# Kernel optimization log

Measured on AMD Instinct MI355X. Metric: run time of the kernel, lower is better.

Reference implementation:

```python
import jax, jax.numpy as jnp
import numpy as np


def _fwht(x):
    """Fast Walsh-Hadamard transform along the last axis (length must be 2^k)."""
    orig_shape = x.shape
    n = orig_shape[-1]
    x = x.reshape(-1, n)
    h = 1
    while h < n:
        # split last dim into (n // (2h), 2, h) blocks and do the butterfly
        x = x.reshape(-1, n // (2 * h), 2, h)
        a = x[:, :, 0, :]
        b = x[:, :, 1, :]
        x = jnp.stack([a + b, a - b], axis=2).reshape(-1, n)
        h *= 2
    return x.reshape(orig_shape)


def setup_inputs() -> dict:
    key = jax.random.key(0)
    x = jax.random.normal(key, (16384, 4096), dtype=jnp.float32)
    scale = jnp.ones((), dtype=jnp.float32)
    return {"x": x, "scale": scale}


def reference(x, scale):
    # Faithful to fwht(input, scale): Hadamard butterfly then scalar scale.
    return _fwht(x) * scale
```

## Files before the change

kernel.cpp:

```cpp
#include <hip/hip_runtime.h>


#define SJ 68
#define SC 1096
#define LDS_WORDS (3 * SC + 15 * SJ + 64)

__global__ __launch_bounds__(64) void fwht_kernel(
    const float* __restrict__ x, const float* __restrict__ scale,
    float* __restrict__ out) {
  __shared__ float lds[LDS_WORDS];
  const int t = threadIdx.x;
  const int row = blockIdx.x;
  const float* xr = x + (size_t)row * 4096;
  float* outr = out + (size_t)row * 4096;

  float v[16][4];
#pragma unroll
  for (int j = 0; j < 16; ++j) {
    const float4 f = *reinterpret_cast<const float4*>(xr + j * 256 + 4 * t);
    v[j][0] = f.x; v[j][1] = f.y; v[j][2] = f.z; v[j][3] = f.w;
  }

#pragma unroll
  for (int j = 0; j < 16; ++j) {
    {
      float a = v[j][0], b = v[j][1];
      v[j][0] = a + b; v[j][1] = a - b;
      float a2 = v[j][2], b2 = v[j][3];
      v[j][2] = a2 + b2; v[j][3] = a2 - b2;
    }
    {
      float a = v[j][0], b = v[j][2];
      v[j][0] = a + b; v[j][2] = a - b;
      float a2 = v[j][1], b2 = v[j][3];
      v[j][1] = a2 + b2; v[j][3] = a2 - b2;
    }
  }

#pragma unroll
  for (int bit = 0; bit < 4; ++bit) {
    const int mask = 1 << bit;
#pragma unroll
    for (int j = 0; j < 16; ++j) {
      if (!(j & mask)) {
        const int k = j | mask;
#pragma unroll
        for (int c = 0; c < 4; ++c) {
          float a = v[j][c], b = v[k][c];
          v[j][c] = a + b; v[k][c] = a - b;
        }
      }
    }
  }

#pragma unroll
  for (int j = 0; j < 16; ++j) {
#pragma unroll
    for (int c = 0; c < 4; ++c) {
      lds[t + j * SJ + c * SC] = v[j][c];
    }
  }

  __syncthreads();

  const int jp = t >> 2, cp = t & 3;
  const int rbase = jp * SJ + cp * SC;
  float w[64];
#pragma unroll
  for (int k = 0; k < 16; ++k) {
    const float4 f = *reinterpret_cast<const float4*>(&lds[rbase + 4 * k]);
    w[4 * k + 0] = f.x; w[4 * k + 1] = f.y;
    w[4 * k + 2] = f.z; w[4 * k + 3] = f.w;
  }

#pragma unroll
  for (int bit = 0; bit < 6; ++bit) {
    const int mask = 1 << bit;
#pragma unroll
    for (int m = 0; m < 64; ++m) {
      if (!(m & mask)) {
        const int k = m | mask;
        float a = w[m], b = w[k];
        w[m] = a + b; w[k] = a - b;
      }
    }
  }

  const float s = scale[0];
  float* ob = outr + jp * 256 + cp;
#pragma unroll
  for (int m = 0; m < 64; ++m) {
    ob[4 * m] = w[m] * s;
  }
}

extern "C" void kernel_launch(void* const* d_in, const int* in_sizes, int n_in,
                              void* d_out, int out_size, void* d_ws, size_t ws_size,
                              hipStream_t stream) {
  const float* x = (const float*)d_in[0];
  const float* scale = (const float*)d_in[1];
  float* out = (float*)d_out;
  const int rows = 16384;
  fwht_kernel<<<rows, 64, 0, stream>>>(x, scale, out);
}
```

Before: 457.3 us.

## Use 256 threads per row with two LDS transpose stages

Each row is now processed by 256 threads holding 16 values each instead of 64 threads holding 64 values. A second LDS exchange stage with padded strides and an extra barrier splits the transform into three 4-bit passes. This cuts register pressure and should raise occupancy and memory-level parallelism for a bandwidth-bound kernel. The cost is more LDS traffic and an extra synchronization per row.

```diff
diff --git a/kernel.cpp b/kernel.cpp
--- a/kernel.cpp
+++ b/kernel.cpp
@@ -1,105 +1,91 @@
 #include <hip/hip_runtime.h>
 
 
-#define SJ 68
-#define SC 1096
-#define LDS_WORDS (3 * SC + 15 * SJ + 64)
+__device__ __forceinline__ void bfly(float& a, float& b) {
+  const float x = a, y = b;
+  a = x + y;
+  b = x - y;
+}
 
-__global__ __launch_bounds__(64) void fwht_kernel(
+__global__ __launch_bounds__(256, 8) void fwht_kernel(
     const float* __restrict__ x, const float* __restrict__ scale,
     float* __restrict__ out) {
-  __shared__ float lds[LDS_WORDS];
+  __shared__ __align__(16) float lds[4348];
   const int t = threadIdx.x;
   const int row = blockIdx.x;
   const float* xr = x + (size_t)row * 4096;
   float* outr = out + (size_t)row * 4096;
+  const float s = scale[0];
 
-  float v[16][4];
+  float r[16];
+
 #pragma unroll
-  for (int j = 0; j < 16; ++j) {
-    const float4 f = *reinterpret_cast<const float4*>(xr + j * 256 + 4 * t);
-    v[j][0] = f.x; v[j][1] = f.y; v[j][2] = f.z; v[j][3] = f.w;
+  for (int k = 0; k < 4; ++k) {
+    const float4 f = *reinterpret_cast<const float4*>(xr + k * 1024 + 4 * t);
+    r[k * 4 + 0] = f.x; r[k * 4 + 1] = f.y;
+    r[k * 4 + 2] = f.z; r[k * 4 + 3] = f.w;
   }
 
 #pragma unroll
-  for (int j = 0; j < 16; ++j) {
-    {
-      float a = v[j][0], b = v[j][1];
-      v[j][0] = a + b; v[j][1] = a - b;
-      float a2 = v[j][2], b2 = v[j][3];
-      v[j][2] = a2 + b2; v[j][3] = a2 - b2;
-    }
-    {
-      float a = v[j][0], b = v[j][2];
-      v[j][0] = a + b; v[j][2] = a - b;
-      float a2 = v[j][1], b2 = v[j][3];
-      v[j][1] = a2 + b2; v[j][3] = a2 - b2;
+  for (int k = 0; k < 4; ++k) {
+    bfly(r[k * 4 + 0], r[k * 4 + 1]); bfly(r[k * 4 + 2], r[k * 4 + 3]);
+    bfly(r[k * 4 + 0], r[k * 4 + 2]); bfly(r[k * 4 + 1], r[k * 4 + 3]);
+  }
+#pragma unroll
+  for (int c = 0; c < 4; ++c) {
+    bfly(r[0 + c], r[4 + c]); bfly(r[8 + c], r[12 + c]);
+    bfly(r[0 + c], r[8 + c]); bfly(r[4 + c], r[12 + c]);
+  }
+
+  {
+    const int wb = 4 * t + 4 * (t >> 4);
+#pragma unroll
+    for (int k = 0; k < 4; ++k) {
+      *reinterpret_cast<float4*>(&lds[k * 1088 + wb]) =
+          make_float4(r[k * 4 + 0], r[k * 4 + 1], r[k * 4 + 2], r[k * 4 + 3]);
     }
   }
+  __syncthreads();
+
+  const int rb1 = (t >> 2) * 68 + (t & 3);
+#pragma unroll
+  for (int m = 0; m < 16; ++m) r[m] = lds[rb1 + 4 * m];
 
 #pragma unroll
   for (int bit = 0; bit < 4; ++bit) {
     const int mask = 1 << bit;
 #pragma unroll
-    for (int j = 0; j < 16; ++j) {
-      if (!(j & mask)) {
-        const int k = j | mask;
-#pragma unroll
-        for (int c = 0; c < 4; ++c) {
-          float a = v[j][c], b = v[k][c];
-          v[j][c] = a + b; v[k][c] = a - b;
-        }
-      }
-    }
+    for (int m = 0; m < 16; ++m)
+      if (!(m & mask)) bfly(r[m], r[m | mask]);
   }
 
 #pragma unroll
-  for (int j = 0; j < 16; ++j) {
+  for (int m = 0; m < 16; ++m) lds[rb1 + 4 * m] = r[m];
+  __syncthreads();
+
+  const int rb2 = (t >> 6) * 1088 + (t & 63);
 #pragma unroll
-    for (int c = 0; c < 4; ++c) {
-      lds[t + j * SJ + c * SC] = v[j][c];
-    }
+  for (int g = 0; g < 16; ++g) r[g] = lds[rb2 + 68 * g];
+
+#pragma unroll
+  for (int bit = 0; bit < 4; ++bit) {
+    const int mask = 1 << bit;
+#pragma unroll
+    for (int g = 0; g < 16; ++g)
+      if (!(g & mask)) bfly(r[g], r[g | mask]);
   }
 
-  __syncthreads();
-
-  const int jp = t >> 2, cp = t & 3;
-  const int rbase = jp * SJ + cp * SC;
-  float w[64];
+  float* op = outr + (t >> 6) * 1024 + (t & 63);
 #pragma unroll
-  for (int k = 0; k < 16; ++k) {
-    const float4 f = *reinterpret_cast<const float4*>(&lds[rbase + 4 * k]);
-    w[4 * k + 0] = f.x; w[4 * k + 1] = f.y;
-    w[4 * k + 2] = f.z; w[4 * k + 3] = f.w;
-  }
-
-#pragma unroll
-  for (int bit = 0; bit < 6; ++bit) {
-    const int mask = 1 << bit;
-#pragma unroll
-    for (int m = 0; m < 64; ++m) {
-      if (!(m & mask)) {
-        const int k = m | mask;
-        float a = w[m], b = w[k];
-        w[m] = a + b; w[k] = a - b;
-      }
-    }
-  }
-
-  const float s = scale[0];
-  float* ob = outr + jp * 256 + cp;
-#pragma unroll
-  for (int m = 0; m < 64; ++m) {
-    ob[4 * m] = w[m] * s;
-  }
+  for (int g = 0; g < 16; ++g) op[g * 64] = r[g] * s;
 }
 
 extern "C" void kernel_launch(void* const* d_in, const int* in_sizes, int n_in,
                               void* d_out, int out_size, void* d_ws, size_t ws_size,
                               hipStream_t stream) {
+  (void)in_sizes; (void)n_in; (void)d_ws; (void)ws_size; (void)out_size;
   const float* x = (const float*)d_in[0];
   const float* scale = (const float*)d_in[1];
   float* out = (float*)d_out;
-  const int rows = 16384;
-  fwht_kernel<<<rows, 64, 0, stream>>>(x, scale, out);
+  fwht_kernel<<<16384, 256, 0, stream>>>(x, scale, out);
 }
```

New measurement: 425.8 us. 6.9% less time.
